# Performance work log

Measured on AMD Instinct MI355X. Metric: run time of the kernel, lower is better.

## Reference

```python
import jax, jax.numpy as jnp
import numpy as np

N = 100000        # nodes
E = 1600000       # directed edges (avg degree 16)
F_IN, F_HID, F_OUT = 512, 32, 16


def setup_inputs() -> dict:
    key = jax.random.key(0)
    k0, k1, k2, k3 = jax.random.split(key, 4)
    x = jax.random.normal(k0, (N, F_IN), dtype=jnp.float32)
    edge_index = jax.random.randint(k1, (2, E), 0, N, dtype=jnp.int32)
    # Glorot-ish init for the two GCNConv linear weights
    W1 = jax.random.normal(k2, (F_IN, F_HID), dtype=jnp.float32) / np.float32(np.sqrt(F_IN))
    W2 = jax.random.normal(k3, (F_HID, F_OUT), dtype=jnp.float32) / np.float32(np.sqrt(F_HID))
    b1 = jnp.zeros((F_HID,), jnp.float32)
    b2 = jnp.zeros((F_OUT,), jnp.float32)
    return {"x": x, "W1": W1, "b1": b1, "W2": W2, "b2": b2, "edge_index": edge_index}


def gcn_conv(x, W, b, src, dst):
    """PyG GCNConv: h = x W; symmetric-normalized aggregation with self-loops; + bias."""
    h = x @ W                                   # [N, F_out] project first (PyG order)
    # degree including the implicit self-loop (start from ones)
    deg = jnp.ones((N,), h.dtype).at[dst].add(1.0)
    dinv = jax.lax.rsqrt(deg)                   # deg^{-1/2}
    coef = (dinv[src] * dinv[dst])[:, None]     # [E, 1] edge norm
    msg = h[src] * coef                         # gather + scale
    agg = jax.ops.segment_sum(msg, dst, num_segments=N)  # scatter-add to dst
    agg = agg + h * (dinv * dinv)[:, None]      # self-loop contribution
    return agg + b


def reference(x, W1, b1, W2, b2, edge_index):
    src, dst = edge_index[0], edge_index[1]
    h = jax.nn.relu(gcn_conv(x, W1, b1, src, dst))
    # F.dropout(training=self.training) is identity in eval mode
    h = gcn_conv(h, W2, b2, src, dst)
    return jax.nn.log_softmax(h, axis=1)
```

## Files before the change

kernel.cpp:

```cpp
#include <hip/hip_runtime.h>
#include <hip/hip_bf16.h>
#include <cstdint>

#define NN   100000
#define NE   1600000
#define FIN  512
#define FHID 32
#define FOUT 16

#define BSHIFT 8
#define BSIZE  256
#define NBUCK  391
#define EPB    2048
#define NCHUNK ((NE + EPB - 1) / EPB)

typedef float f32x4 __attribute__((ext_vector_type(4)));
typedef short s16x8 __attribute__((ext_vector_type(8)));
typedef short s16x4 __attribute__((ext_vector_type(4)));
typedef int   i32x4 __attribute__((ext_vector_type(4)));
typedef unsigned int u32;
typedef unsigned short u16;

__device__ __forceinline__ short f2bf(float f) {
  union { float f; uint32_t u; } v; v.f = f;
  uint32_t r = v.u + 0x7fffu + ((v.u >> 16) & 1u);
  return (short)(r >> 16);
}
__device__ __forceinline__ float bf2f(u16 u) {
  union { uint32_t u; float f; } v; v.u = (uint32_t)u << 16; return v.f;
}

__global__ __launch_bounds__(256) void k_hist(const int* __restrict__ dst,
                                              u32* __restrict__ bcount) {
  __shared__ u32 h[NBUCK];
  int tid = threadIdx.x;
  for (int i = tid; i < NBUCK; i += 256) h[i] = 0;
  __syncthreads();
  int base = blockIdx.x * EPB;
  #pragma unroll
  for (int i = 0; i < 2; ++i) {
    int e0 = base + (i * 256 + tid) * 4;
    if (e0 + 3 < NE) {
      i32x4 d4 = *(const i32x4*)(dst + e0);
      atomicAdd(&h[d4[0] >> BSHIFT], 1u);
      atomicAdd(&h[d4[1] >> BSHIFT], 1u);
      atomicAdd(&h[d4[2] >> BSHIFT], 1u);
      atomicAdd(&h[d4[3] >> BSHIFT], 1u);
    } else {
      for (int k = 0; k < 4; ++k)
        if (e0 + k < NE) atomicAdd(&h[dst[e0 + k] >> BSHIFT], 1u);
    }
  }
  __syncthreads();
  for (int i = tid; i < NBUCK; i += 256)
    if (h[i]) atomicAdd(&bcount[i], h[i]);
}

__global__ __launch_bounds__(512) void k_bscan(const u32* __restrict__ bc,
                                               u32* __restrict__ bstart,
                                               u32* __restrict__ bcur) {
  __shared__ u32 tmp[512];
  int tid = threadIdx.x;
  u32 v = (tid < NBUCK) ? bc[tid] : 0;
  tmp[tid] = v;
  __syncthreads();
  #pragma unroll
  for (int off = 1; off < 512; off <<= 1) {
    u32 t = (tid >= off) ? tmp[tid - off] : 0;
    __syncthreads();
    tmp[tid] += t;
    __syncthreads();
  }
  if (tid < NBUCK) { u32 e = tmp[tid] - v; bstart[tid] = e; bcur[tid] = e; }
  if (tid == 511) bstart[NBUCK] = tmp[511];
}

__global__ __launch_bounds__(512) void k_bin(const int* __restrict__ src,
                                             const int* __restrict__ dst,
                                             u32* __restrict__ bcur,
                                             u32* __restrict__ binned) {
  __shared__ u32 cnt[NBUCK];
  __shared__ u32 lofs[NBUCK];
  __shared__ u32 gbase[NBUCK];
  __shared__ u32 tmp[512];
  __shared__ u32 stage[EPB];
  __shared__ u16 sb[EPB];
  int tid = threadIdx.x;
  for (int i = tid; i < NBUCK; i += 512) cnt[i] = 0;
  __syncthreads();

  int base = blockIdx.x * EPB;
  int e0 = base + tid * 4;
  u32 vals[4];
  u32 ofs[4];
  int bks[4];
  if (e0 + 3 < NE) {
    i32x4 s4 = *(const i32x4*)(src + e0);
    i32x4 d4 = *(const i32x4*)(dst + e0);
    #pragma unroll
    for (int k = 0; k < 4; ++k) {
      int b = d4[k] >> BSHIFT;
      bks[k] = b;
      vals[k] = (u32)s4[k] | ((u32)(d4[k] & (BSIZE - 1)) << 17);
      ofs[k] = atomicAdd(&cnt[b], 1u);
    }
  } else {
    #pragma unroll
    for (int k = 0; k < 4; ++k) {
      int e = e0 + k;
      bool ok = e < NE;
      int s = 0, d = 0;
      if (ok) { s = src[e]; d = dst[e]; }
      int b = ok ? (d >> BSHIFT) : -1;
      bks[k] = b;
      vals[k] = (u32)s | ((u32)(d & (BSIZE - 1)) << 17);
      ofs[k] = ok ? atomicAdd(&cnt[b], 1u) : 0;
    }
  }
  __syncthreads();

  u32 cv = (tid < NBUCK) ? cnt[tid] : 0;
  tmp[tid] = cv;
  __syncthreads();
  #pragma unroll
  for (int off = 1; off < 512; off <<= 1) {
    u32 t = (tid >= off) ? tmp[tid - off] : 0;
    __syncthreads();
    tmp[tid] += t;
    __syncthreads();
  }
  if (tid < NBUCK) {
    lofs[tid] = tmp[tid] - cv;
    gbase[tid] = cv ? atomicAdd(&bcur[tid], cv) : 0;
  }
  __syncthreads();
  u32 total = tmp[511];
  __syncthreads();

  #pragma unroll
  for (int k = 0; k < 4; ++k) {
    if (bks[k] >= 0) {
      u32 sl = lofs[bks[k]] + ofs[k];
      stage[sl] = vals[k];
      sb[sl] = (u16)bks[k];
    }
  }
  __syncthreads();

  for (u32 s2 = tid; s2 < total; s2 += 512) {
    int b = sb[s2];
    binned[gbase[b] + (s2 - lofs[b])] = stage[s2];
  }
}

__global__ __launch_bounds__(256) void k_fin(const u32* __restrict__ binned,
                                             const u32* __restrict__ bstart,
                                             int* __restrict__ deg,
                                             int* __restrict__ rs,
                                             float* __restrict__ dinv,
                                             int* __restrict__ csr) {
  __shared__ u32 degl[BSIZE];
  __shared__ u32 rsl[BSIZE];
  int tid = threadIdx.x;
  int b = blockIdx.x;
  u32 start = bstart[b];
  u32 n = bstart[b + 1] - start;

  degl[tid] = 0;
  __syncthreads();
  for (u32 k = tid; k < n; k += 256)
    atomicAdd(&degl[binned[start + k] >> 17], 1u);
  __syncthreads();

  u32 v = degl[tid];
  rsl[tid] = v;
  __syncthreads();
  #pragma unroll
  for (int off = 1; off < 256; off <<= 1) {
    u32 t = (tid >= off) ? rsl[tid - off] : 0;
    __syncthreads();
    rsl[tid] += t;
    __syncthreads();
  }
  u32 e = rsl[tid] - v;
  __syncthreads();
  rsl[tid] = e;

  int g = b * BSIZE + tid;
  if (g < NN) {
    deg[g] = (int)v;
    rs[g] = (int)(start + e);
    dinv[g] = rsqrtf(1.0f + (float)v);
  }
  __syncthreads();

  for (u32 k = tid; k < n; k += 256) {
    u32 vv = binned[start + k];
    u32 pos = atomicAdd(&rsl[vv >> 17], 1u);
    csr[start + pos] = (int)(vv & 0x1FFFFu);
  }
}

__global__ __launch_bounds__(256) void k_gemm1(const float* __restrict__ x,
                                               const float* __restrict__ W1,
                                               const float* __restrict__ dinv,
                                               u16* __restrict__ Hs1) {
  __shared__ s16x8 Blds[16][2][64];
  const int tid = threadIdx.x;
  for (int it = 0; it < 64; ++it) {
    int flat = it * 256 + tid;
    int i  = flat & 7;
    int l  = (flat >> 3) & 63;
    int nt = (flat >> 9) & 1;
    int kt = flat >> 10;
    int k  = kt * 32 + ((l >> 4) << 3) + i;
    int n  = nt * 16 + (l & 15);
    ((short*)Blds)[flat] = f2bf(W1[k * 32 + n]);
  }
  __syncthreads();

  const int lane = tid & 63;
  const int wv   = tid >> 6;
  const int h    = lane >> 4;
  const int m    = lane & 15;
  const int wid  = blockIdx.x * 4 + wv;
  if (wid >= 3125) return;
  const int t0 = wid * 2;

  const float* xr0 = x + (size_t)(t0 * 16 + m) * FIN + h * 8;
  const float* xr1 = xr0 + (size_t)16 * FIN;

  f32x4 acc[2][2] = {};
  #pragma unroll
  for (int kt = 0; kt < 16; ++kt) {
    f32x4 a0 = *(const f32x4*)(xr0 + kt * 32);
    f32x4 a1 = *(const f32x4*)(xr0 + kt * 32 + 4);
    f32x4 c0 = *(const f32x4*)(xr1 + kt * 32);
    f32x4 c1 = *(const f32x4*)(xr1 + kt * 32 + 4);
    s16x8 b0 = Blds[kt][0][lane];
    s16x8 b1 = Blds[kt][1][lane];
    s16x8 af, cf;
    af[0]=f2bf(a0[0]); af[1]=f2bf(a0[1]); af[2]=f2bf(a0[2]); af[3]=f2bf(a0[3]);
    af[4]=f2bf(a1[0]); af[5]=f2bf(a1[1]); af[6]=f2bf(a1[2]); af[7]=f2bf(a1[3]);
    cf[0]=f2bf(c0[0]); cf[1]=f2bf(c0[1]); cf[2]=f2bf(c0[2]); cf[3]=f2bf(c0[3]);
    cf[4]=f2bf(c1[0]); cf[5]=f2bf(c1[1]); cf[6]=f2bf(c1[2]); cf[7]=f2bf(c1[3]);
    acc[0][0] = __builtin_amdgcn_mfma_f32_16x16x32_bf16(af, b0, acc[0][0], 0, 0, 0);
    acc[0][1] = __builtin_amdgcn_mfma_f32_16x16x32_bf16(af, b1, acc[0][1], 0, 0, 0);
    acc[1][0] = __builtin_amdgcn_mfma_f32_16x16x32_bf16(cf, b0, acc[1][0], 0, 0, 0);
    acc[1][1] = __builtin_amdgcn_mfma_f32_16x16x32_bf16(cf, b1, acc[1][1], 0, 0, 0);
  }
  #pragma unroll
  for (int rt = 0; rt < 2; ++rt) {
    #pragma unroll
    for (int r = 0; r < 4; ++r) {
      int row = (t0 + rt) * 16 + h * 4 + r;
      float di = dinv[row];
      u16* o = Hs1 + (size_t)row * FHID + m;
      o[0]  = (u16)f2bf(acc[rt][0][r] * di);
      o[16] = (u16)f2bf(acc[rt][1][r] * di);
    }
  }
}

__global__ __launch_bounds__(256) void k_gat1(const int* __restrict__ csr,
                                              const int* __restrict__ rs,
                                              const int* __restrict__ deg,
                                              const float* __restrict__ dinv,
                                              const float* __restrict__ b1,
                                              const float* __restrict__ W2,
                                              const u16* __restrict__ Hs1,
                                              u16* __restrict__ Hs2) {
  __shared__ float w[FHID * FOUT];
  for (int i = threadIdx.x; i < FHID * FOUT; i += 256) w[i] = W2[i];
  __syncthreads();

  int t = blockIdx.x * 256 + threadIdx.x;
  int d = t >> 2;
  if (d >= NN) return;
  int p = t & 3;
  int start = rs[d], n = deg[d];

  float a0[8], a1[8], a2[8], a3[8];
  {
    s16x8 v = *(const s16x8*)(Hs1 + (size_t)d * FHID + p * 8);
    #pragma unroll
    for (int k = 0; k < 8; ++k) {
      a0[k] = bf2f((u16)v[k]); a1[k] = 0.f; a2[k] = 0.f; a3[k] = 0.f;
    }
  }
  int j = 0;
  for (; j + 8 <= n; j += 8) {
    int s0 = csr[start + j];
    int s1 = csr[start + j + 1];
    int s2 = csr[start + j + 2];
    int s3 = csr[start + j + 3];
    int s4 = csr[start + j + 4];
    int s5 = csr[start + j + 5];
    int s6 = csr[start + j + 6];
    int s7 = csr[start + j + 7];
    s16x8 v0 = *(const s16x8*)(Hs1 + (size_t)s0 * FHID + p * 8);
    s16x8 v1 = *(const s16x8*)(Hs1 + (size_t)s1 * FHID + p * 8);
    s16x8 v2 = *(const s16x8*)(Hs1 + (size_t)s2 * FHID + p * 8);
    s16x8 v3 = *(const s16x8*)(Hs1 + (size_t)s3 * FHID + p * 8);
    s16x8 v4 = *(const s16x8*)(Hs1 + (size_t)s4 * FHID + p * 8);
    s16x8 v5 = *(const s16x8*)(Hs1 + (size_t)s5 * FHID + p * 8);
    s16x8 v6 = *(const s16x8*)(Hs1 + (size_t)s6 * FHID + p * 8);
    s16x8 v7 = *(const s16x8*)(Hs1 + (size_t)s7 * FHID + p * 8);
    #pragma unroll
    for (int k = 0; k < 8; ++k) {
      a0[k] += bf2f((u16)v0[k]);
      a1[k] += bf2f((u16)v1[k]);
      a2[k] += bf2f((u16)v2[k]);
      a3[k] += bf2f((u16)v3[k]);
      a0[k] += bf2f((u16)v4[k]);
      a1[k] += bf2f((u16)v5[k]);
      a2[k] += bf2f((u16)v6[k]);
      a3[k] += bf2f((u16)v7[k]);
    }
  }
  for (; j + 4 <= n; j += 4) {
    int s0 = csr[start + j];
    int s1 = csr[start + j + 1];
    int s2 = csr[start + j + 2];
    int s3 = csr[start + j + 3];
    s16x8 v0 = *(const s16x8*)(Hs1 + (size_t)s0 * FHID + p * 8);
    s16x8 v1 = *(const s16x8*)(Hs1 + (size_t)s1 * FHID + p * 8);
    s16x8 v2 = *(const s16x8*)(Hs1 + (size_t)s2 * FHID + p * 8);
    s16x8 v3 = *(const s16x8*)(Hs1 + (size_t)s3 * FHID + p * 8);
    #pragma unroll
    for (int k = 0; k < 8; ++k) {
      a0[k] += bf2f((u16)v0[k]);
      a1[k] += bf2f((u16)v1[k]);
      a2[k] += bf2f((u16)v2[k]);
      a3[k] += bf2f((u16)v3[k]);
    }
  }
  for (; j < n; ++j) {
    int s0 = csr[start + j];
    s16x8 v0 = *(const s16x8*)(Hs1 + (size_t)s0 * FHID + p * 8);
    #pragma unroll
    for (int k = 0; k < 8; ++k) a0[k] += bf2f((u16)v0[k]);
  }

  float dd = dinv[d];
  float h[8];
  #pragma unroll
  for (int k = 0; k < 8; ++k)
    h[k] = fmaxf(((a0[k] + a1[k]) + (a2[k] + a3[k])) * dd + b1[p * 8 + k], 0.0f);

  float pj[FOUT];
  #pragma unroll
  for (int jj = 0; jj < FOUT; ++jj) pj[jj] = 0.f;
  #pragma unroll
  for (int k = 0; k < 8; ++k)
    #pragma unroll
    for (int jj = 0; jj < FOUT; ++jj)
      pj[jj] = fmaf(h[k], w[(p * 8 + k) * FOUT + jj], pj[jj]);
  #pragma unroll
  for (int jj = 0; jj < FOUT; ++jj) {
    pj[jj] += __shfl_xor(pj[jj], 1);
    pj[jj] += __shfl_xor(pj[jj], 2);
  }
  s16x4 o;
  #pragma unroll
  for (int q = 0; q < 4; ++q) o[q] = f2bf(pj[p * 4 + q] * dd);
  *(s16x4*)(Hs2 + (size_t)d * FOUT + p * 4) = o;
}

__global__ __launch_bounds__(256) void k_gat2(const int* __restrict__ csr,
                                              const int* __restrict__ rs,
                                              const int* __restrict__ deg,
                                              const float* __restrict__ dinv,
                                              const float* __restrict__ b2,
                                              const u16* __restrict__ Hs2,
                                              float* __restrict__ out) {
  int t = blockIdx.x * 256 + threadIdx.x;
  int d = t >> 2;
  if (d >= NN) return;
  int p = t & 3;
  int start = rs[d], n = deg[d];

  float a0[4], a1[4], a2[4], a3[4];
  {
    s16x4 v = *(const s16x4*)(Hs2 + (size_t)d * FOUT + p * 4);
    #pragma unroll
    for (int k = 0; k < 4; ++k) {
      a0[k] = bf2f((u16)v[k]); a1[k] = 0.f; a2[k] = 0.f; a3[k] = 0.f;
    }
  }
  int j = 0;
  for (; j + 8 <= n; j += 8) {
    int s0 = csr[start + j];
    int s1 = csr[start + j + 1];
    int s2 = csr[start + j + 2];
    int s3 = csr[start + j + 3];
    int s4 = csr[start + j + 4];
    int s5 = csr[start + j + 5];
    int s6 = csr[start + j + 6];
    int s7 = csr[start + j + 7];
    s16x4 v0 = *(const s16x4*)(Hs2 + (size_t)s0 * FOUT + p * 4);
    s16x4 v1 = *(const s16x4*)(Hs2 + (size_t)s1 * FOUT + p * 4);
    s16x4 v2 = *(const s16x4*)(Hs2 + (size_t)s2 * FOUT + p * 4);
    s16x4 v3 = *(const s16x4*)(Hs2 + (size_t)s3 * FOUT + p * 4);
    s16x4 v4 = *(const s16x4*)(Hs2 + (size_t)s4 * FOUT + p * 4);
    s16x4 v5 = *(const s16x4*)(Hs2 + (size_t)s5 * FOUT + p * 4);
    s16x4 v6 = *(const s16x4*)(Hs2 + (size_t)s6 * FOUT + p * 4);
    s16x4 v7 = *(const s16x4*)(Hs2 + (size_t)s7 * FOUT + p * 4);
    #pragma unroll
    for (int k = 0; k < 4; ++k) {
      a0[k] += bf2f((u16)v0[k]);
      a1[k] += bf2f((u16)v1[k]);
      a2[k] += bf2f((u16)v2[k]);
      a3[k] += bf2f((u16)v3[k]);
      a0[k] += bf2f((u16)v4[k]);
      a1[k] += bf2f((u16)v5[k]);
      a2[k] += bf2f((u16)v6[k]);
      a3[k] += bf2f((u16)v7[k]);
    }
  }
  for (; j + 4 <= n; j += 4) {
    int s0 = csr[start + j];
    int s1 = csr[start + j + 1];
    int s2 = csr[start + j + 2];
    int s3 = csr[start + j + 3];
    s16x4 v0 = *(const s16x4*)(Hs2 + (size_t)s0 * FOUT + p * 4);
    s16x4 v1 = *(const s16x4*)(Hs2 + (size_t)s1 * FOUT + p * 4);
    s16x4 v2 = *(const s16x4*)(Hs2 + (size_t)s2 * FOUT + p * 4);
    s16x4 v3 = *(const s16x4*)(Hs2 + (size_t)s3 * FOUT + p * 4);
    #pragma unroll
    for (int k = 0; k < 4; ++k) {
      a0[k] += bf2f((u16)v0[k]);
      a1[k] += bf2f((u16)v1[k]);
      a2[k] += bf2f((u16)v2[k]);
      a3[k] += bf2f((u16)v3[k]);
    }
  }
  for (; j < n; ++j) {
    int s0 = csr[start + j];
    s16x4 v0 = *(const s16x4*)(Hs2 + (size_t)s0 * FOUT + p * 4);
    #pragma unroll
    for (int k = 0; k < 4; ++k) a0[k] += bf2f((u16)v0[k]);
  }

  float dd = dinv[d];
  float z[4];
  #pragma unroll
  for (int k = 0; k < 4; ++k)
    z[k] = ((a0[k] + a1[k]) + (a2[k] + a3[k])) * dd + b2[p * 4 + k];

  float m = fmaxf(fmaxf(z[0], z[1]), fmaxf(z[2], z[3]));
  m = fmaxf(m, __shfl_xor(m, 1));
  m = fmaxf(m, __shfl_xor(m, 2));
  float s = expf(z[0]-m) + expf(z[1]-m) + expf(z[2]-m) + expf(z[3]-m);
  s += __shfl_xor(s, 1);
  s += __shfl_xor(s, 2);
  float lse = m + logf(s);

  f32x4 o = { z[0]-lse, z[1]-lse, z[2]-lse, z[3]-lse };
  *(f32x4*)(out + (size_t)d * FOUT + p * 4) = o;
}

extern "C" void kernel_launch(void* const* d_in, const int* in_sizes, int n_in,
                              void* d_out, int out_size, void* d_ws, size_t ws_size,
                              hipStream_t stream) {
  const float* x  = (const float*)d_in[0];
  const float* W1 = (const float*)d_in[1];
  const float* b1 = (const float*)d_in[2];
  const float* W2 = (const float*)d_in[3];
  const float* b2 = (const float*)d_in[4];
  const int*   ei = (const int*)d_in[5];
  const int* srcv = ei;
  const int* dstv = ei + NE;

  char* ws = (char*)d_ws;
  const size_t KB = 1024, MB = 1048576;
  u32*   bcount = (u32*)(ws + 0);
  u32*   bstart = (u32*)(ws + 8 * KB);
  u32*   bcur   = (u32*)(ws + 16 * KB);
  int*   deg    = (int*)(ws + 512 * KB);
  int*   rs     = (int*)(ws + 1024 * KB);
  float* dinv   = (float*)(ws + 1536 * KB);
  u32*   binned = (u32*)(ws + 2 * MB);
  int*   csr    = (int*)(ws + 9 * MB);
  u16*   Hs1    = (u16*)(ws + 16 * MB);
  u16*   Hs2    = (u16*)(ws + 23 * MB);
  float* out    = (float*)d_out;

  hipMemsetAsync(bcount, 0, NBUCK * sizeof(u32), stream);

  k_hist <<<NCHUNK, 256, 0, stream>>>(dstv, bcount);
  k_bscan<<<1,      512, 0, stream>>>(bcount, bstart, bcur);
  k_bin  <<<NCHUNK, 512, 0, stream>>>(srcv, dstv, bcur, binned);
  k_fin  <<<NBUCK,  256, 0, stream>>>(binned, bstart, deg, rs, dinv, csr);
  k_gemm1<<<782, 256, 0, stream>>>(x, W1, dinv, Hs1);
  k_gat1 <<<(NN * 4 + 255) / 256, 256, 0, stream>>>(csr, rs, deg, dinv, b1, W2, Hs1, Hs2);
  k_gat2 <<<(NN * 4 + 255) / 256, 256, 0, stream>>>(csr, rs, deg, dinv, b2, Hs2, out);
}
```

Baseline: 164.3 us.

## Fuse histogram and bucket scan into GEMM kernel, defer source-side dinv scaling

```diff
diff --git a/kernel.cpp b/kernel.cpp
--- a/kernel.cpp
+++ b/kernel.cpp
@@ -11,8 +11,9 @@
 #define BSHIFT 8
 #define BSIZE  256
 #define NBUCK  391
-#define EPB    2048
-#define NCHUNK ((NE + EPB - 1) / EPB)
+#define BEPB   2048
+#define NBB    ((NE + BEPB - 1) / BEPB)
+#define GEMMB  782
 
 typedef float f32x4 __attribute__((ext_vector_type(4)));
 typedef short s16x8 __attribute__((ext_vector_type(8)));
@@ -30,49 +31,130 @@
   union { uint32_t u; float f; } v; v.u = (uint32_t)u << 16; return v.f;
 }
 
-__global__ __launch_bounds__(256) void k_hist(const int* __restrict__ dst,
-                                              u32* __restrict__ bcount) {
-  __shared__ u32 h[NBUCK];
-  int tid = threadIdx.x;
-  for (int i = tid; i < NBUCK; i += 256) h[i] = 0;
-  __syncthreads();
-  int base = blockIdx.x * EPB;
-  #pragma unroll
-  for (int i = 0; i < 2; ++i) {
-    int e0 = base + (i * 256 + tid) * 4;
-    if (e0 + 3 < NE) {
-      i32x4 d4 = *(const i32x4*)(dst + e0);
-      atomicAdd(&h[d4[0] >> BSHIFT], 1u);
-      atomicAdd(&h[d4[1] >> BSHIFT], 1u);
-      atomicAdd(&h[d4[2] >> BSHIFT], 1u);
-      atomicAdd(&h[d4[3] >> BSHIFT], 1u);
-    } else {
-      for (int k = 0; k < 4; ++k)
-        if (e0 + k < NE) atomicAdd(&h[dst[e0 + k] >> BSHIFT], 1u);
+union GemmSh {
+  s16x8 B[16][2][64];
+  struct { u32 h[NBUCK]; u32 wsum[8]; } hs;
+};
+__global__ __launch_bounds__(256) void k_gemm1(
+    const float* __restrict__ x, const float* __restrict__ W1,
+    const int* __restrict__ dst,
+    u32* __restrict__ bcount, u32* __restrict__ ticket,
+    u32* __restrict__ bstart, u32* __restrict__ bcur,
+    u16* __restrict__ H1) {
+  __shared__ GemmSh sh;
+  __shared__ bool amlast;
+  const int tid = threadIdx.x;
+  const int lane64 = tid & 63;
+
+  for (int i = tid; i < NBUCK; i += 256) sh.hs.h[i] = 0;
+  __syncthreads();
+  {
+    int base = blockIdx.x * BEPB;
+    #pragma unroll
+    for (int i = 0; i < 2; ++i) {
+      int e0 = base + (i * 256 + tid) * 4;
+      if (e0 + 3 < NE) {
+        i32x4 d4 = *(const i32x4*)(dst + e0);
+        atomicAdd(&sh.hs.h[d4[0] >> BSHIFT], 1u);
+        atomicAdd(&sh.hs.h[d4[1] >> BSHIFT], 1u);
+        atomicAdd(&sh.hs.h[d4[2] >> BSHIFT], 1u);
+        atomicAdd(&sh.hs.h[d4[3] >> BSHIFT], 1u);
+      } else {
+        for (int k = 0; k < 4; ++k)
+          if (e0 + k < NE) atomicAdd(&sh.hs.h[dst[e0 + k] >> BSHIFT], 1u);
+      }
     }
   }
   __syncthreads();
   for (int i = tid; i < NBUCK; i += 256)
-    if (h[i]) atomicAdd(&bcount[i], h[i]);
-}
-
-__global__ __launch_bounds__(512) void k_bscan(const u32* __restrict__ bc,
-                                               u32* __restrict__ bstart,
-                                               u32* __restrict__ bcur) {
-  __shared__ u32 tmp[512];
-  int tid = threadIdx.x;
-  u32 v = (tid < NBUCK) ? bc[tid] : 0;
-  tmp[tid] = v;
-  __syncthreads();
-  #pragma unroll
-  for (int off = 1; off < 512; off <<= 1) {
-    u32 t = (tid >= off) ? tmp[tid - off] : 0;
+    if (sh.hs.h[i]) atomicAdd(&bcount[i], sh.hs.h[i]);
+  __syncthreads();
+  if (tid == 0) {
+    __threadfence();
+    u32 t = __hip_atomic_fetch_add(ticket, 1u, __ATOMIC_ACQ_REL, __HIP_MEMORY_SCOPE_AGENT);
+    amlast = (t == gridDim.x - 1);
+  }
+  __syncthreads();
+  if (amlast) {
+    u32 a0 = (2*tid   < NBUCK) ? __hip_atomic_load(&bcount[2*tid],   __ATOMIC_RELAXED, __HIP_MEMORY_SCOPE_AGENT) : 0;
+    u32 a1 = (2*tid+1 < NBUCK) ? __hip_atomic_load(&bcount[2*tid+1], __ATOMIC_RELAXED, __HIP_MEMORY_SCOPE_AGENT) : 0;
+    u32 s = a0 + a1;
+    u32 v = s;
+    #pragma unroll
+    for (int off = 1; off < 64; off <<= 1) {
+      u32 t = __shfl_up(v, off);
+      if (lane64 >= off) v += t;
+    }
+    if (lane64 == 63) sh.hs.wsum[tid >> 6] = v;
     __syncthreads();
-    tmp[tid] += t;
+    if (tid < 4) {
+      u32 w0 = sh.hs.wsum[tid], w = w0;
+      #pragma unroll
+      for (int off = 1; off < 4; off <<= 1) {
+        u32 t = __shfl_up(w, off, 4);
+        if ((tid & 3) >= off) w += t;
+      }
+      sh.hs.wsum[tid] = w - w0;
+    }
     __syncthreads();
-  }
-  if (tid < NBUCK) { u32 e = tmp[tid] - v; bstart[tid] = e; bcur[tid] = e; }
-  if (tid == 511) bstart[NBUCK] = tmp[511];
+    u32 excl = v - s + sh.hs.wsum[tid >> 6];
+    if (2*tid < NBUCK)     { bstart[2*tid]   = excl;      bcur[2*tid]   = excl; }
+    if (2*tid+1 < NBUCK)   { bstart[2*tid+1] = excl + a0; bcur[2*tid+1] = excl + a0; }
+    if (tid == 255) bstart[NBUCK] = excl + s;
+    __syncthreads();
+  }
+
+  for (int it = 0; it < 64; ++it) {
+    int flat = it * 256 + tid;
+    int i  = flat & 7;
+    int l  = (flat >> 3) & 63;
+    int nt = (flat >> 9) & 1;
+    int kt = flat >> 10;
+    int k  = kt * 32 + ((l >> 4) << 3) + i;
+    int n  = nt * 16 + (l & 15);
+    ((short*)sh.B)[flat] = f2bf(W1[k * 32 + n]);
+  }
+  __syncthreads();
+
+  const int wv = tid >> 6;
+  const int h  = lane64 >> 4;
+  const int m  = lane64 & 15;
+  const int wid = blockIdx.x * 4 + wv;
+  if (wid >= 3125) return;
+  const int t0 = wid * 2;
+
+  const float* xr0 = x + (size_t)(t0 * 16 + m) * FIN + h * 8;
+  const float* xr1 = xr0 + (size_t)16 * FIN;
+
+  f32x4 acc[2][2] = {};
+  #pragma unroll
+  for (int kt = 0; kt < 16; ++kt) {
+    f32x4 a0 = *(const f32x4*)(xr0 + kt * 32);
+    f32x4 a1 = *(const f32x4*)(xr0 + kt * 32 + 4);
+    f32x4 c0 = *(const f32x4*)(xr1 + kt * 32);
+    f32x4 c1 = *(const f32x4*)(xr1 + kt * 32 + 4);
+    s16x8 b0 = sh.B[kt][0][lane64];
+    s16x8 b1 = sh.B[kt][1][lane64];
+    s16x8 af, cf;
+    af[0]=f2bf(a0[0]); af[1]=f2bf(a0[1]); af[2]=f2bf(a0[2]); af[3]=f2bf(a0[3]);
+    af[4]=f2bf(a1[0]); af[5]=f2bf(a1[1]); af[6]=f2bf(a1[2]); af[7]=f2bf(a1[3]);
+    cf[0]=f2bf(c0[0]); cf[1]=f2bf(c0[1]); cf[2]=f2bf(c0[2]); cf[3]=f2bf(c0[3]);
+    cf[4]=f2bf(c1[0]); cf[5]=f2bf(c1[1]); cf[6]=f2bf(c1[2]); cf[7]=f2bf(c1[3]);
+    acc[0][0] = __builtin_amdgcn_mfma_f32_16x16x32_bf16(af, b0, acc[0][0], 0, 0, 0);
+    acc[0][1] = __builtin_amdgcn_mfma_f32_16x16x32_bf16(af, b1, acc[0][1], 0, 0, 0);
+    acc[1][0] = __builtin_amdgcn_mfma_f32_16x16x32_bf16(cf, b0, acc[1][0], 0, 0, 0);
+    acc[1][1] = __builtin_amdgcn_mfma_f32_16x16x32_bf16(cf, b1, acc[1][1], 0, 0, 0);
+  }
+  #pragma unroll
+  for (int rt = 0; rt < 2; ++rt) {
+    #pragma unroll
+    for (int r = 0; r < 4; ++r) {
+      int row = (t0 + rt) * 16 + h * 4 + r;
+      u16* o = H1 + (size_t)row * FHID + m;
+      o[0]  = (u16)f2bf(acc[rt][0][r]);
+      o[16] = (u16)f2bf(acc[rt][1][r]);
+    }
+  }
 }
 
 __global__ __launch_bounds__(512) void k_bin(const int* __restrict__ src,
@@ -82,18 +164,18 @@
   __shared__ u32 cnt[NBUCK];
   __shared__ u32 lofs[NBUCK];
   __shared__ u32 gbase[NBUCK];
-  __shared__ u32 tmp[512];
-  __shared__ u32 stage[EPB];
-  __shared__ u16 sb[EPB];
+  __shared__ u32 wsum[8];
+  __shared__ u32 sh_total;
+  __shared__ u32 stage[BEPB];
+  __shared__ u16 sb[BEPB];
   int tid = threadIdx.x;
+  int lane = tid & 63;
   for (int i = tid; i < NBUCK; i += 512) cnt[i] = 0;
   __syncthreads();
 
-  int base = blockIdx.x * EPB;
+  int base = blockIdx.x * BEPB;
   int e0 = base + tid * 4;
-  u32 vals[4];
-  u32 ofs[4];
-  int bks[4];
+  u32 vals[4]; u32 ofs[4]; int bks[4];
   if (e0 + 3 < NE) {
     i32x4 s4 = *(const i32x4*)(src + e0);
     i32x4 d4 = *(const i32x4*)(dst + e0);
@@ -119,23 +201,33 @@
   }
   __syncthreads();
 
-  u32 cv = (tid < NBUCK) ? cnt[tid] : 0;
-  tmp[tid] = cv;
-  __syncthreads();
-  #pragma unroll
-  for (int off = 1; off < 512; off <<= 1) {
-    u32 t = (tid >= off) ? tmp[tid - off] : 0;
-    __syncthreads();
-    tmp[tid] += t;
-    __syncthreads();
-  }
+  u32 orig = (tid < NBUCK) ? cnt[tid] : 0;
+  u32 v = orig;
+  #pragma unroll
+  for (int off = 1; off < 64; off <<= 1) {
+    u32 t = __shfl_up(v, off);
+    if (lane >= off) v += t;
+  }
+  if (lane == 63) wsum[tid >> 6] = v;
+  __syncthreads();
+  if (tid < 8) {
+    u32 w0 = wsum[tid], w = w0;
+    #pragma unroll
+    for (int off = 1; off < 8; off <<= 1) {
+      u32 t = __shfl_up(w, off, 8);
+      if ((tid & 7) >= off) w += t;
+    }
+    wsum[tid] = w - w0;
+  }
+  __syncthreads();
+  u32 excl = v - orig + wsum[tid >> 6];
   if (tid < NBUCK) {
-    lofs[tid] = tmp[tid] - cv;
-    gbase[tid] = cv ? atomicAdd(&bcur[tid], cv) : 0;
-  }
-  __syncthreads();
-  u32 total = tmp[511];
-  __syncthreads();
+    lofs[tid] = excl;
+    gbase[tid] = orig ? atomicAdd(&bcur[tid], orig) : 0;
+  }
+  if (tid == 511) sh_total = excl + orig;
+  __syncthreads();
+  u32 total = sh_total;
 
   #pragma unroll
   for (int k = 0; k < 4; ++k) {
@@ -161,7 +253,9 @@
                                              int* __restrict__ csr) {
   __shared__ u32 degl[BSIZE];
   __shared__ u32 rsl[BSIZE];
+  __shared__ u32 wsum[4];
   int tid = threadIdx.x;
+  int lane = tid & 63;
   int b = blockIdx.x;
   u32 start = bstart[b];
   u32 n = bstart[b + 1] - start;
@@ -172,25 +266,33 @@
     atomicAdd(&degl[binned[start + k] >> 17], 1u);
   __syncthreads();
 
-  u32 v = degl[tid];
-  rsl[tid] = v;
-  __syncthreads();
-  #pragma unroll
-  for (int off = 1; off < 256; off <<= 1) {
-    u32 t = (tid >= off) ? rsl[tid - off] : 0;
-    __syncthreads();
-    rsl[tid] += t;
-    __syncthreads();
-  }
-  u32 e = rsl[tid] - v;
-  __syncthreads();
-  rsl[tid] = e;
+  u32 orig = degl[tid];
+  u32 v = orig;
+  #pragma unroll
+  for (int off = 1; off < 64; off <<= 1) {
+    u32 t = __shfl_up(v, off);
+    if (lane >= off) v += t;
+  }
+  if (lane == 63) wsum[tid >> 6] = v;
+  __syncthreads();
+  if (tid < 4) {
+    u32 w0 = wsum[tid], w = w0;
+    #pragma unroll
+    for (int off = 1; off < 4; off <<= 1) {
+      u32 t = __shfl_up(w, off, 4);
+      if ((tid & 3) >= off) w += t;
+    }
+    wsum[tid] = w - w0;
+  }
+  __syncthreads();
+  u32 excl = v - orig + wsum[tid >> 6];
+  rsl[tid] = excl;
 
   int g = b * BSIZE + tid;
   if (g < NN) {
-    deg[g] = (int)v;
-    rs[g] = (int)(start + e);
-    dinv[g] = rsqrtf(1.0f + (float)v);
+    deg[g] = (int)orig;
+    rs[g] = (int)(start + excl);
+    dinv[g] = rsqrtf(1.0f + (float)orig);
   }
   __syncthreads();
 
@@ -198,67 +300,6 @@
     u32 vv = binned[start + k];
     u32 pos = atomicAdd(&rsl[vv >> 17], 1u);
     csr[start + pos] = (int)(vv & 0x1FFFFu);
-  }
-}
-
-__global__ __launch_bounds__(256) void k_gemm1(const float* __restrict__ x,
-                                               const float* __restrict__ W1,
-                                               const float* __restrict__ dinv,
-                                               u16* __restrict__ Hs1) {
-  __shared__ s16x8 Blds[16][2][64];
-  const int tid = threadIdx.x;
-  for (int it = 0; it < 64; ++it) {
-    int flat = it * 256 + tid;
-    int i  = flat & 7;
-    int l  = (flat >> 3) & 63;
-    int nt = (flat >> 9) & 1;
-    int kt = flat >> 10;
-    int k  = kt * 32 + ((l >> 4) << 3) + i;
-    int n  = nt * 16 + (l & 15);
-    ((short*)Blds)[flat] = f2bf(W1[k * 32 + n]);
-  }
-  __syncthreads();
-
-  const int lane = tid & 63;
-  const int wv   = tid >> 6;
-  const int h    = lane >> 4;
-  const int m    = lane & 15;
-  const int wid  = blockIdx.x * 4 + wv;
-  if (wid >= 3125) return;
-  const int t0 = wid * 2;
-
-  const float* xr0 = x + (size_t)(t0 * 16 + m) * FIN + h * 8;
-  const float* xr1 = xr0 + (size_t)16 * FIN;
-
-  f32x4 acc[2][2] = {};
-  #pragma unroll
-  for (int kt = 0; kt < 16; ++kt) {
-    f32x4 a0 = *(const f32x4*)(xr0 + kt * 32);
-    f32x4 a1 = *(const f32x4*)(xr0 + kt * 32 + 4);
-    f32x4 c0 = *(const f32x4*)(xr1 + kt * 32);
-    f32x4 c1 = *(const f32x4*)(xr1 + kt * 32 + 4);
-    s16x8 b0 = Blds[kt][0][lane];
-    s16x8 b1 = Blds[kt][1][lane];
-    s16x8 af, cf;
-    af[0]=f2bf(a0[0]); af[1]=f2bf(a0[1]); af[2]=f2bf(a0[2]); af[3]=f2bf(a0[3]);
-    af[4]=f2bf(a1[0]); af[5]=f2bf(a1[1]); af[6]=f2bf(a1[2]); af[7]=f2bf(a1[3]);
-    cf[0]=f2bf(c0[0]); cf[1]=f2bf(c0[1]); cf[2]=f2bf(c0[2]); cf[3]=f2bf(c0[3]);
-    cf[4]=f2bf(c1[0]); cf[5]=f2bf(c1[1]); cf[6]=f2bf(c1[2]); cf[7]=f2bf(c1[3]);
-    acc[0][0] = __builtin_amdgcn_mfma_f32_16x16x32_bf16(af, b0, acc[0][0], 0, 0, 0);
-    acc[0][1] = __builtin_amdgcn_mfma_f32_16x16x32_bf16(af, b1, acc[0][1], 0, 0, 0);
-    acc[1][0] = __builtin_amdgcn_mfma_f32_16x16x32_bf16(cf, b0, acc[1][0], 0, 0, 0);
-    acc[1][1] = __builtin_amdgcn_mfma_f32_16x16x32_bf16(cf, b1, acc[1][1], 0, 0, 0);
-  }
-  #pragma unroll
-  for (int rt = 0; rt < 2; ++rt) {
-    #pragma unroll
-    for (int r = 0; r < 4; ++r) {
-      int row = (t0 + rt) * 16 + h * 4 + r;
-      float di = dinv[row];
-      u16* o = Hs1 + (size_t)row * FHID + m;
-      o[0]  = (u16)f2bf(acc[rt][0][r] * di);
-      o[16] = (u16)f2bf(acc[rt][1][r] * di);
-    }
   }
 }
 
@@ -268,7 +309,7 @@
                                               const float* __restrict__ dinv,
                                               const float* __restrict__ b1,
                                               const float* __restrict__ W2,
-                                              const u16* __restrict__ Hs1,
+                                              const u16* __restrict__ H1,
                                               u16* __restrict__ Hs2) {
   __shared__ float w[FHID * FOUT];
   for (int i = threadIdx.x; i < FHID * FOUT; i += 256) w[i] = W2[i];
@@ -279,70 +320,65 @@
   if (d >= NN) return;
   int p = t & 3;
   int start = rs[d], n = deg[d];
+  float dd = dinv[d];
 
   float a0[8], a1[8], a2[8], a3[8];
   {
-    s16x8 v = *(const s16x8*)(Hs1 + (size_t)d * FHID + p * 8);
+    s16x8 v = *(const s16x8*)(H1 + (size_t)d * FHID + p * 8);
     #pragma unroll
     for (int k = 0; k < 8; ++k) {
-      a0[k] = bf2f((u16)v[k]); a1[k] = 0.f; a2[k] = 0.f; a3[k] = 0.f;
+      a0[k] = dd * bf2f((u16)v[k]); a1[k] = 0.f; a2[k] = 0.f; a3[k] = 0.f;
     }
   }
   int j = 0;
   for (; j + 8 <= n; j += 8) {
-    int s0 = csr[start + j];
-    int s1 = csr[start + j + 1];
-    int s2 = csr[start + j + 2];
-    int s3 = csr[start + j + 3];
-    int s4 = csr[start + j + 4];
-    int s5 = csr[start + j + 5];
-    int s6 = csr[start + j + 6];
-    int s7 = csr[start + j + 7];
-    s16x8 v0 = *(const s16x8*)(Hs1 + (size_t)s0 * FHID + p * 8);
-    s16x8 v1 = *(const s16x8*)(Hs1 + (size_t)s1 * FHID + p * 8);
-    s16x8 v2 = *(const s16x8*)(Hs1 + (size_t)s2 * FHID + p * 8);
-    s16x8 v3 = *(const s16x8*)(Hs1 + (size_t)s3 * FHID + p * 8);
-    s16x8 v4 = *(const s16x8*)(Hs1 + (size_t)s4 * FHID + p * 8);
-    s16x8 v5 = *(const s16x8*)(Hs1 + (size_t)s5 * FHID + p * 8);
-    s16x8 v6 = *(const s16x8*)(Hs1 + (size_t)s6 * FHID + p * 8);
-    s16x8 v7 = *(const s16x8*)(Hs1 + (size_t)s7 * FHID + p * 8);
+    int s0=csr[start+j],   s1=csr[start+j+1], s2=csr[start+j+2], s3=csr[start+j+3];
+    int s4=csr[start+j+4], s5=csr[start+j+5], s6=csr[start+j+6], s7=csr[start+j+7];
+    float d0=dinv[s0], d1=dinv[s1], d2=dinv[s2], d3=dinv[s3];
+    float d4=dinv[s4], d5=dinv[s5], d6=dinv[s6], d7=dinv[s7];
+    s16x8 v0 = *(const s16x8*)(H1 + (size_t)s0 * FHID + p * 8);
+    s16x8 v1 = *(const s16x8*)(H1 + (size_t)s1 * FHID + p * 8);
+    s16x8 v2 = *(const s16x8*)(H1 + (size_t)s2 * FHID + p * 8);
+    s16x8 v3 = *(const s16x8*)(H1 + (size_t)s3 * FHID + p * 8);
+    s16x8 v4 = *(const s16x8*)(H1 + (size_t)s4 * FHID + p * 8);
+    s16x8 v5 = *(const s16x8*)(H1 + (size_t)s5 * FHID + p * 8);
+    s16x8 v6 = *(const s16x8*)(H1 + (size_t)s6 * FHID + p * 8);
+    s16x8 v7 = *(const s16x8*)(H1 + (size_t)s7 * FHID + p * 8);
     #pragma unroll
     for (int k = 0; k < 8; ++k) {
-      a0[k] += bf2f((u16)v0[k]);
-      a1[k] += bf2f((u16)v1[k]);
-      a2[k] += bf2f((u16)v2[k]);
-      a3[k] += bf2f((u16)v3[k]);
-      a0[k] += bf2f((u16)v4[k]);
-      a1[k] += bf2f((u16)v5[k]);
-      a2[k] += bf2f((u16)v6[k]);
-      a3[k] += bf2f((u16)v7[k]);
+      a0[k] = fmaf(d0, bf2f((u16)v0[k]), a0[k]);
+      a1[k] = fmaf(d1, bf2f((u16)v1[k]), a1[k]);
+      a2[k] = fmaf(d2, bf2f((u16)v2[k]), a2[k]);
+      a3[k] = fmaf(d3, bf2f((u16)v3[k]), a3[k]);
+      a0[k] = fmaf(d4, bf2f((u16)v4[k]), a0[k]);
+      a1[k] = fmaf(d5, bf2f((u16)v5[k]), a1[k]);
+      a2[k] = fmaf(d6, bf2f((u16)v6[k]), a2[k]);
+      a3[k] = fmaf(d7, bf2f((u16)v7[k]), a3[k]);
     }
   }
   for (; j + 4 <= n; j += 4) {
-    int s0 = csr[start + j];
-    int s1 = csr[start + j + 1];
-    int s2 = csr[start + j + 2];
-    int s3 = csr[start + j + 3];
-    s16x8 v0 = *(const s16x8*)(Hs1 + (size_t)s0 * FHID + p * 8);
-    s16x8 v1 = *(const s16x8*)(Hs1 + (size_t)s1 * FHID + p * 8);
-    s16x8 v2 = *(const s16x8*)(Hs1 + (size_t)s2 * FHID + p * 8);
-    s16x8 v3 = *(const s16x8*)(Hs1 + (size_t)s3 * FHID + p * 8);
+    int s0=csr[start+j], s1=csr[start+j+1], s2=csr[start+j+2], s3=csr[start+j+3];
+    float d0=dinv[s0], d1=dinv[s1], d2=dinv[s2], d3=dinv[s3];
+    s16x8 v0 = *(const s16x8*)(H1 + (size_t)s0 * FHID + p * 8);
+    s16x8 v1 = *(const s16x8*)(H1 + (size_t)s1 * FHID + p * 8);
+    s16x8 v2 = *(const s16x8*)(H1 + (size_t)s2 * FHID + p * 8);
+    s16x8 v3 = *(const s16x8*)(H1 + (size_t)s3 * FHID + p * 8);
     #pragma unroll
     for (int k = 0; k < 8; ++k) {
-      a0[k] += bf2f((u16)v0[k]);
-      a1[k] += bf2f((u16)v1[k]);
-      a2[k] += bf2f((u16)v2[k]);
-      a3[k] += bf2f((u16)v3[k]);
+      a0[k] = fmaf(d0, bf2f((u16)v0[k]), a0[k]);
+      a1[k] = fmaf(d1, bf2f((u16)v1[k]), a1[k]);
+      a2[k] = fmaf(d2, bf2f((u16)v2[k]), a2[k]);
+      a3[k] = fmaf(d3, bf2f((u16)v3[k]), a3[k]);
     }
   }
   for (; j < n; ++j) {
     int s0 = csr[start + j];
-    s16x8 v0 = *(const s16x8*)(Hs1 + (size_t)s0 * FHID + p * 8);
-    #pragma unroll
-    for (int k = 0; k < 8; ++k) a0[k] += bf2f((u16)v0[k]);
-  }
-
-  float dd = dinv[d];
+    float d0 = dinv[s0];
+    s16x8 v0 = *(const s16x8*)(H1 + (size_t)s0 * FHID + p * 8);
+    #pragma unroll
+    for (int k = 0; k < 8; ++k) a0[k] = fmaf(d0, bf2f((u16)v0[k]), a0[k]);
+  }
+
   float h[8];
   #pragma unroll
   for (int k = 0; k < 8; ++k)
@@ -384,20 +420,12 @@
   {
     s16x4 v = *(const s16x4*)(Hs2 + (size_t)d * FOUT + p * 4);
     #pragma unroll
-    for (int k = 0; k < 4; ++k) {
-      a0[k] = bf2f((u16)v[k]); a1[k] = 0.f; a2[k] = 0.f; a3[k] = 0.f;
-    }
+    for (int k = 0; k < 4; ++k) { a0[k] = bf2f((u16)v[k]); a1[k]=0.f; a2[k]=0.f; a3[k]=0.f; }
   }
   int j = 0;
   for (; j + 8 <= n; j += 8) {
-    int s0 = csr[start + j];
-    int s1 = csr[start + j + 1];
-    int s2 = csr[start + j + 2];
-    int s3 = csr[start + j + 3];
-    int s4 = csr[start + j + 4];
-    int s5 = csr[start + j + 5];
-    int s6 = csr[start + j + 6];
-    int s7 = csr[start + j + 7];
+    int s0=csr[start+j],   s1=csr[start+j+1], s2=csr[start+j+2], s3=csr[start+j+3];
+    int s4=csr[start+j+4], s5=csr[start+j+5], s6=csr[start+j+6], s7=csr[start+j+7];
     s16x4 v0 = *(const s16x4*)(Hs2 + (size_t)s0 * FOUT + p * 4);
     s16x4 v1 = *(const s16x4*)(Hs2 + (size_t)s1 * FOUT + p * 4);
     s16x4 v2 = *(const s16x4*)(Hs2 + (size_t)s2 * FOUT + p * 4);
@@ -408,31 +436,22 @@
     s16x4 v7 = *(const s16x4*)(Hs2 + (size_t)s7 * FOUT + p * 4);
     #pragma unroll
     for (int k = 0; k < 4; ++k) {
-      a0[k] += bf2f((u16)v0[k]);
-      a1[k] += bf2f((u16)v1[k]);
-      a2[k] += bf2f((u16)v2[k]);
-      a3[k] += bf2f((u16)v3[k]);
-      a0[k] += bf2f((u16)v4[k]);
-      a1[k] += bf2f((u16)v5[k]);
-      a2[k] += bf2f((u16)v6[k]);
-      a3[k] += bf2f((u16)v7[k]);
+      a0[k] += bf2f((u16)v0[k]); a1[k] += bf2f((u16)v1[k]);
+      a2[k] += bf2f((u16)v2[k]); a3[k] += bf2f((u16)v3[k]);
+      a0[k] += bf2f((u16)v4[k]); a1[k] += bf2f((u16)v5[k]);
+      a2[k] += bf2f((u16)v6[k]); a3[k] += bf2f((u16)v7[k]);
     }
   }
   for (; j + 4 <= n; j += 4) {
-    int s0 = csr[start + j];
-    int s1 = csr[start + j + 1];
-    int s2 = csr[start + j + 2];
-    int s3 = csr[start + j + 3];
+    int s0=csr[start+j], s1=csr[start+j+1], s2=csr[start+j+2], s3=csr[start+j+3];
     s16x4 v0 = *(const s16x4*)(Hs2 + (size_t)s0 * FOUT + p * 4);
     s16x4 v1 = *(const s16x4*)(Hs2 + (size_t)s1 * FOUT + p * 4);
     s16x4 v2 = *(const s16x4*)(Hs2 + (size_t)s2 * FOUT + p * 4);
     s16x4 v3 = *(const s16x4*)(Hs2 + (size_t)s3 * FOUT + p * 4);
     #pragma unroll
     for (int k = 0; k < 4; ++k) {
-      a0[k] += bf2f((u16)v0[k]);
-      a1[k] += bf2f((u16)v1[k]);
-      a2[k] += bf2f((u16)v2[k]);
-      a3[k] += bf2f((u16)v3[k]);
+      a0[k] += bf2f((u16)v0[k]); a1[k] += bf2f((u16)v1[k]);
+      a2[k] += bf2f((u16)v2[k]); a3[k] += bf2f((u16)v3[k]);
     }
   }
   for (; j < n; ++j) {
@@ -446,7 +465,7 @@
   float z[4];
   #pragma unroll
   for (int k = 0; k < 4; ++k)
-    z[k] = ((a0[k] + a1[k]) + (a2[k] + a3[k])) * dd + b2[p * 4 + k];
+    z[k] = ((a0[k]+a1[k]) + (a2[k]+a3[k])) * dd + b2[p * 4 + k];
 
   float m = fmaxf(fmaxf(z[0], z[1]), fmaxf(z[2], z[3]));
   m = fmaxf(m, __shfl_xor(m, 1));
@@ -475,6 +494,7 @@
   char* ws = (char*)d_ws;
   const size_t KB = 1024, MB = 1048576;
   u32*   bcount = (u32*)(ws + 0);
+  u32*   ticket = (u32*)(ws + 1600);
   u32*   bstart = (u32*)(ws + 8 * KB);
   u32*   bcur   = (u32*)(ws + 16 * KB);
   int*   deg    = (int*)(ws + 512 * KB);
@@ -482,17 +502,15 @@
   float* dinv   = (float*)(ws + 1536 * KB);
   u32*   binned = (u32*)(ws + 2 * MB);
   int*   csr    = (int*)(ws + 9 * MB);
-  u16*   Hs1    = (u16*)(ws + 16 * MB);
+  u16*   H1     = (u16*)(ws + 16 * MB);
   u16*   Hs2    = (u16*)(ws + 23 * MB);
   float* out    = (float*)d_out;
 
-  hipMemsetAsync(bcount, 0, NBUCK * sizeof(u32), stream);
-
-  k_hist <<<NCHUNK, 256, 0, stream>>>(dstv, bcount);
-  k_bscan<<<1,      512, 0, stream>>>(bcount, bstart, bcur);
-  k_bin  <<<NCHUNK, 512, 0, stream>>>(srcv, dstv, bcur, binned);
-  k_fin  <<<NBUCK,  256, 0, stream>>>(binned, bstart, deg, rs, dinv, csr);
-  k_gemm1<<<782, 256, 0, stream>>>(x, W1, dinv, Hs1);
-  k_gat1 <<<(NN * 4 + 255) / 256, 256, 0, stream>>>(csr, rs, deg, dinv, b1, W2, Hs1, Hs2);
+  hipMemsetAsync(ws, 0, 2 * KB, stream);
+
+  k_gemm1<<<GEMMB, 256, 0, stream>>>(x, W1, dstv, bcount, ticket, bstart, bcur, H1);
+  k_bin  <<<NBB, 512, 0, stream>>>(srcv, dstv, bcur, binned);
+  k_fin  <<<NBUCK, 256, 0, stream>>>(binned, bstart, deg, rs, dinv, csr);
+  k_gat1 <<<(NN * 4 + 255) / 256, 256, 0, stream>>>(csr, rs, deg, dinv, b1, W2, H1, Hs2);
   k_gat2 <<<(NN * 4 + 255) / 256, 256, 0, stream>>>(csr, rs, deg, dinv, b2, Hs2, out);
 }
```

New measurement: 178.6 us. 1.09x slower.
